# Kernel optimization log

Hardware: AMD Instinct MI355X
Metric: run time of the kernel (lower is better)

Reference implementation:

```python
import jax, jax.numpy as jnp
import numpy as np
import math

PS = 8          # patch_size
OUT_C = 16      # out_channels
D_MODEL = 64
P_STATE = 32
BANDLIMIT = 1.0
STEP_SCALE = 1.0  # dt1 reference rate


def _ln(x, g, b, eps=1e-5):
    mu = jnp.mean(x, -1, keepdims=True)
    var = jnp.mean((x - mu) ** 2, -1, keepdims=True)
    return (x - mu) * jax.lax.rsqrt(var + eps) * g + b


def _forward(x, W_embed, b_embed, g1, beta1, Lambda_re, Lambda_im, B_re, B_im,
             C_re, C_im, D, log_step, g2, beta2, W_enc, W_dec, g3, beta3, W_out, b_out):
    b, t, h, w = x.shape
    hp, wp = h // PS, w // PS
    n = hp * wp
    # patchify: [b,t,h,w] -> [b,t,n,ps*ps]
    xp = x.reshape(b, t, hp, PS, wp, PS).transpose(0, 1, 2, 4, 3, 5).reshape(b, t, n, PS * PS)
    xe = xp @ W_embed.T + b_embed                              # [b,t,n,d]
    u = xe.transpose(0, 2, 1, 3).reshape(b * n, t, D_MODEL)    # [(b n), t, d]

    # ---- S5Block: pre-norm -> diagonal SSM -> gelu + residual -> GEGLU FFN ----
    fx = _ln(u, g1, beta1)
    Lam = Lambda_re + 1j * Lambda_im                           # [P] complex eigenvalues
    step = STEP_SCALE * jnp.exp(log_step)                      # [P]
    Lbar = jnp.exp(Lam * step)                                 # ZOH: A_bar
    Bbar = ((Lbar - 1.0) / Lam)[:, None] * (B_re + 1j * B_im)  # ZOH: B_bar [P,d]
    # bandlimit mask on C (freqs = step*|Im(Lambda)|/(2pi) < bandlimit/2)
    freqs = step * jnp.abs(Lambda_im) / (2.0 * math.pi)
    mask = (freqs < BANDLIMIT * 0.5).astype(C_re.dtype)
    Cc = (C_re + 1j * C_im) * mask[None, :]                    # [d,P]

    Bu = jnp.einsum('ntd,pd->ntp', fx.astype(jnp.complex64), Bbar)   # [(bn),t,P]
    A = jnp.broadcast_to(Lbar.astype(jnp.complex64), (1, t, P_STATE))

    def comb(e1, e2):
        a1, b1 = e1
        a2, b2 = e2
        return a1 * a2, a2 * b1 + b2

    _, xs = jax.lax.associative_scan(comb, (A, Bu), axis=1)    # x_k = A*x_{k-1} + Bu_k (x_0 = 0)
    ys = jnp.einsum('ntp,dp->ntd', xs, Cc).real + fx * D       # y = Re(C x) + D u
    xb = jax.nn.gelu(ys, approximate=False) + fx

    fx2 = _ln(xb, g2, beta2)
    enc = fx2 @ W_enc.T                                        # [(bn),t,2d]
    a, gate = jnp.split(enc, 2, axis=-1)
    xb = (a * jax.nn.gelu(gate, approximate=False)) @ W_dec.T + fx2

    # ---- take last timestep, project, unpatchify ----
    x_last = xb[:, -1, :]                                      # [(bn), d]
    proj = _ln(x_last, g3, beta3) @ W_out.T + b_out            # [(bn), C*ps*ps]
    y = proj.reshape(b, hp, wp, OUT_C, PS, PS).transpose(0, 3, 1, 4, 2, 5).reshape(b, OUT_C, h, w)
    return y


def setup_inputs() -> dict:
    key = jax.random.key(0)
    ks = jax.random.split(key, 12)
    d, P, pp = D_MODEL, P_STATE, PS * PS
    return dict(
        x=jax.random.normal(ks[0], (8, 15, 480, 640), jnp.float32),
        W_embed=jax.random.normal(ks[1], (d, pp), jnp.float32) / math.sqrt(pp),
        b_embed=jnp.zeros((d,), jnp.float32),
        g1=jnp.ones((d,), jnp.float32), beta1=jnp.zeros((d,), jnp.float32),
        Lambda_re=-0.5 * jnp.ones((P,), jnp.float32),
        Lambda_im=math.pi * (1.0 + jnp.arange(P, dtype=jnp.float32)),
        B_re=jax.random.normal(ks[2], (P, d), jnp.float32) / math.sqrt(d),
        B_im=jax.random.normal(ks[3], (P, d), jnp.float32) / math.sqrt(d),
        C_re=jax.random.normal(ks[4], (d, P), jnp.float32) / math.sqrt(P),
        C_im=jax.random.normal(ks[5], (d, P), jnp.float32) / math.sqrt(P),
        D=jax.random.normal(ks[6], (d,), jnp.float32),
        log_step=jax.random.uniform(ks[7], (P,), jnp.float32, math.log(1e-3), math.log(1e-1)),
        g2=jnp.ones((d,), jnp.float32), beta2=jnp.zeros((d,), jnp.float32),
        W_enc=jax.random.normal(ks[8], (2 * d, d), jnp.float32) / math.sqrt(d),
        W_dec=jax.random.normal(ks[9], (d, d), jnp.float32) / math.sqrt(d),
        g3=jnp.ones((d,), jnp.float32), beta3=jnp.zeros((d,), jnp.float32),
        W_out=jax.random.normal(ks[10], (OUT_C * pp, d), jnp.float32) / math.sqrt(d),
        b_out=jnp.zeros((OUT_C * pp,), jnp.float32),
    )


def reference(x, W_embed, b_embed, g1, beta1, Lambda_re, Lambda_im, B_re, B_im,
              C_re, C_im, D, log_step, g2, beta2, W_enc, W_dec, g3, beta3, W_out, b_out):
    return _forward(x, W_embed, b_embed, g1, beta1, Lambda_re, Lambda_im, B_re, B_im,
                    C_re, C_im, D, log_step, g2, beta2, W_enc, W_dec, g3, beta3, W_out, b_out)
```

## Files before the change

kernel.cpp:

```cpp
#include <hip/hip_runtime.h>
#include <math.h>


typedef __attribute__((ext_vector_type(8))) short short8;
typedef __attribute__((ext_vector_type(4))) float f32x4;

#define MFMA16(a, b, c) __builtin_amdgcn_mfma_f32_16x16x32_bf16((a), (b), (c), 0, 0, 0)

__device__ __forceinline__ short f2bf(float f) {
  union { float f; unsigned u; } v; v.f = f;
  unsigned r = (v.u + 0x7fffu + ((v.u >> 16) & 1u)) >> 16;
  return (short)r;
}
__device__ __forceinline__ float geluf(float x) {
  return 0.5f * x * (1.0f + erff(x * 0.70710678118654752f));
}
__device__ __forceinline__ short8 packfrag(const f32x4& a, const f32x4& b) {
  short8 o;
  o[0] = f2bf(a[0]); o[1] = f2bf(a[1]); o[2] = f2bf(a[2]); o[3] = f2bf(a[3]);
  o[4] = f2bf(b[0]); o[5] = f2bf(b[1]); o[6] = f2bf(b[2]); o[7] = f2bf(b[3]);
  return o;
}
__device__ __forceinline__ int ecmap(int i, int m) {
  return (i >> 1) * 32 + (m >> 2) * 8 + (i & 1) * 4 + (m & 3);
}
__device__ __forceinline__ void bbar_factors(const float* Lre, const float* Lim,
                                             const float* lstep, int p,
                                             float& fre, float& fim) {
  float st = expf(lstep[p]);
  float lr = Lre[p], li = Lim[p];
  float er = expf(lr * st);
  float lbr = er * cosf(li * st), lbi = er * sinf(li * st);
  float u = lbr - 1.0f, v = lbi;
  float den = lr * lr + li * li;
  fre = (u * lr + v * li) / den;
  fim = (v * lr - u * li) / den;
}

__global__ __launch_bounds__(256) void k0_prep(
    const float* __restrict__ W_embed, const float* __restrict__ g1,
    const float* __restrict__ be1, const float* __restrict__ Lre,
    const float* __restrict__ Lim, const float* __restrict__ Bre,
    const float* __restrict__ Bim, const float* __restrict__ Cre,
    const float* __restrict__ Cim, const float* __restrict__ lstep,
    const float* __restrict__ W_enc, const float* __restrict__ W_dec,
    const float* __restrict__ W_out, short* __restrict__ wimg,
    float* __restrict__ bu0) {
  const int bid = blockIdx.x;
  if (bid == 44) {
    int q = threadIdx.x;
    if (q < 64) {
      int c = q >> 5, p = q & 31;
      float fre, fim; bbar_factors(Lre, Lim, lstep, p, fre, fim);
      float s = 0.f;
      for (int d = 0; d < 64; ++d) {
        float br = Bre[p * 64 + d], bi = Bim[p * 64 + d];
        float val = c ? (fre * bi + fim * br) : (fre * br - fim * bi);
        s += be1[d] * val;
      }
      bu0[q] = s;
    }
    return;
  }
  const int w = threadIdx.x >> 6, lane = threadIdx.x & 63;
  const int m = lane & 15, qd = lane >> 4;
  const int f = bid * 4 + w;
  short v[8];
  if (f < 8) {
    int i = f >> 1, kt = f & 1, chan = ecmap(i, m), k0 = kt * 32 + qd * 8;
#pragma unroll
    for (int j = 0; j < 8; ++j) v[j] = f2bf(W_embed[chan * 64 + k0 + j]);
  } else if (f < 16) {
    int fi = f - 8, i = fi >> 1, kt = fi & 1;
    int comp = i & 1, p = (i >> 1) * 16 + m, d0 = kt * 32 + qd * 8;
    float fre, fim; bbar_factors(Lre, Lim, lstep, p, fre, fim);
#pragma unroll
    for (int j = 0; j < 8; ++j) {
      int d = d0 + j;
      float br = Bre[p * 64 + d], bi = Bim[p * 64 + d];
      float val = comp ? (fre * bi + fim * br) : (fre * br - fim * bi);
      v[j] = f2bf(g1[d] * val);
    }
  } else if (f < 24) {
    int fi = f - 16, i = fi >> 1, kt = fi & 1, chan = ecmap(i, m);
#pragma unroll
    for (int j = 0; j < 8; ++j) {
      int comp = j >> 2, p = kt * 16 + qd * 4 + (j & 3);
      float stp = expf(lstep[p]);
      float fr = stp * fabsf(Lim[p]) * (1.0f / 6.28318530717958648f);
      float msk = (fr < 0.5f) ? 1.f : 0.f;
      float val = comp ? -Cim[chan * 32 + p] * msk : Cre[chan * 32 + p] * msk;
      v[j] = f2bf(val);
    }
  } else if (f < 40) {
    int fi = f - 24, i = fi >> 1, kt = fi & 1;
    int row = (i < 4) ? ecmap(i, m) : 64 + ecmap(i - 4, m);
#pragma unroll
    for (int j = 0; j < 8; ++j) v[j] = f2bf(W_enc[row * 64 + kt * 32 + qd * 8 + j]);
  } else if (f < 48) {
    int fi = f - 40, i = fi >> 1, kt = fi & 1, row = ecmap(i, m);
#pragma unroll
    for (int j = 0; j < 8; ++j) v[j] = f2bf(W_dec[row * 64 + kt * 32 + qd * 8 + j]);
  } else {
    int fi = f - 48, i = fi >> 1, kt = fi & 1, row = i * 16 + m;
#pragma unroll
    for (int j = 0; j < 8; ++j) v[j] = f2bf(W_out[row * 64 + kt * 32 + qd * 8 + j]);
  }
  short8 sv;
#pragma unroll
  for (int j = 0; j < 8; ++j) sv[j] = v[j];
  *(short8*)&wimg[(f * 64 + lane) * 8] = sv;
}

__global__ __launch_bounds__(256) void k1_fused(
    const float* __restrict__ x, const short* __restrict__ wimg_g,
    const float* __restrict__ bu0_g, const float* __restrict__ Lre,
    const float* __restrict__ Lim, const float* __restrict__ lstep,
    const float* __restrict__ g1, const float* __restrict__ be1,
    const float* __restrict__ bemb, const float* __restrict__ Dv,
    const float* __restrict__ g2, const float* __restrict__ be2,
    float* __restrict__ xlastT) {
  __shared__ short wimg[48 * 512];
  {
    float4* dst = (float4*)wimg;
    const float4* src = (const float4*)wimg_g;
    for (int i = threadIdx.x; i < 3072; i += 256) dst[i] = src[i];
  }
  __syncthreads();
#define WF(id) (*(const short8*)&wimg[(id) * 512 + lane * 8])

  const int wv = threadIdx.x >> 6, lane = threadIdx.x & 63;
  const int s = lane & 15, qd = lane >> 4;
  const int sbase = (blockIdx.x * 4 + wv) * 16;
  const int b_i = sbase / 4800;
  const int pr = sbase % 4800;
  const int ph = pr / 80;
  const int pw0 = pr % 80;
  const float* xbase = x + ((b_i * 15) * 480 + ph * 8) * 640 + (pw0 + s) * 8;

  int cb[4];
  f32x4 bec[4], bu0c[4];
#pragma unroll
  for (int nt = 0; nt < 4; ++nt) {
    cb[nt] = (nt >> 1) * 32 + qd * 8 + (nt & 1) * 4;
    bec[nt] = *(const f32x4*)(bemb + cb[nt]);
    bu0c[nt] = *(const f32x4*)(bu0_g + (nt & 1) * 32 + (nt >> 1) * 16 + qd * 4);
  }
  f32x4 lbr[2], lbi[2];
#pragma unroll
  for (int k = 0; k < 2; ++k)
#pragma unroll
    for (int r = 0; r < 4; ++r) {
      int p = k * 16 + qd * 4 + r;
      float st = expf(lstep[p]);
      float er = expf(Lre[p] * st);
      lbr[k][r] = er * cosf(Lim[p] * st);
      lbi[k][r] = er * sinf(Lim[p] * st);
    }

  const f32x4 zf = {0.f, 0.f, 0.f, 0.f};
  f32x4 state[4] = {zf, zf, zf, zf};
  f32x4 xh[4];

  f32x4 vcur[4], vnext[4];
#pragma unroll
  for (int kt = 0; kt < 2; ++kt) {
    const float* rp = xbase + (kt * 4 + qd) * 640;
    vcur[kt * 2] = *(const f32x4*)rp;
    vcur[kt * 2 + 1] = *(const f32x4*)(rp + 4);
  }

  for (int t = 0; t < 15; ++t) {
    if (t < 14) {
      const float* xn = xbase + (t + 1) * 307200;
#pragma unroll
      for (int kt = 0; kt < 2; ++kt) {
        const float* rp = xn + (kt * 4 + qd) * 640;
        vnext[kt * 2] = *(const f32x4*)rp;
        vnext[kt * 2 + 1] = *(const f32x4*)(rp + 4);
      }
    }
    short8 pa0 = packfrag(vcur[0], vcur[1]);
    short8 pa1 = packfrag(vcur[2], vcur[3]);
    f32x4 c1[4];
#pragma unroll
    for (int i = 0; i < 4; ++i) {
      f32x4 acc = MFMA16(WF(i * 2), pa0, zf);
      acc = MFMA16(WF(i * 2 + 1), pa1, acc);
      c1[i] = acc + bec[i];
    }
    float sm = 0.f, sq = 0.f;
#pragma unroll
    for (int nt = 0; nt < 4; ++nt)
#pragma unroll
      for (int i = 0; i < 4; ++i) { sm += c1[nt][i]; sq += c1[nt][i] * c1[nt][i]; }
    sm += __shfl_xor(sm, 16); sq += __shfl_xor(sq, 16);
    sm += __shfl_xor(sm, 32); sq += __shfl_xor(sq, 32);
    float mean = sm * 0.015625f;
    float rstd = rsqrtf(sq * 0.015625f - mean * mean + 1e-5f);
#pragma unroll
    for (int nt = 0; nt < 4; ++nt) xh[nt] = (c1[nt] - mean) * rstd;
    short8 xa0 = packfrag(xh[0], xh[1]);
    short8 xa1 = packfrag(xh[2], xh[3]);
#pragma unroll
    for (int k = 0; k < 2; ++k) {
      f32x4 re = state[2 * k], im = state[2 * k + 1];
      state[2 * k]     = lbr[k] * re - lbi[k] * im + bu0c[2 * k];
      state[2 * k + 1] = lbr[k] * im + lbi[k] * re + bu0c[2 * k + 1];
    }
#pragma unroll
    for (int i = 0; i < 4; ++i) {
      state[i] = MFMA16(WF(8 + i * 2), xa0, state[i]);
      state[i] = MFMA16(WF(8 + i * 2 + 1), xa1, state[i]);
    }
#pragma unroll
    for (int q = 0; q < 4; ++q) vcur[q] = vnext[q];
  }

  f32x4 g1c[4], b1c[4], Dc[4], g2c[4], b2c[4];
#pragma unroll
  for (int nt = 0; nt < 4; ++nt) {
    g1c[nt] = *(const f32x4*)(g1 + cb[nt]);
    b1c[nt] = *(const f32x4*)(be1 + cb[nt]);
    Dc[nt] = *(const f32x4*)(Dv + cb[nt]);
    g2c[nt] = *(const f32x4*)(g2 + cb[nt]);
    b2c[nt] = *(const f32x4*)(be2 + cb[nt]);
  }
  f32x4 fxl[4];
#pragma unroll
  for (int nt = 0; nt < 4; ++nt) fxl[nt] = xh[nt] * g1c[nt] + b1c[nt];

  short8 xsa0 = packfrag(state[0], state[1]);
  short8 xsa1 = packfrag(state[2], state[3]);
  f32x4 xbv[4];
#pragma unroll
  for (int i = 0; i < 4; ++i) {
    f32x4 acc = fxl[i] * Dc[i];
    acc = MFMA16(WF(16 + i * 2), xsa0, acc);
    acc = MFMA16(WF(16 + i * 2 + 1), xsa1, acc);
#pragma unroll
    for (int r = 0; r < 4; ++r) xbv[i][r] = geluf(acc[r]) + fxl[i][r];
  }
  float sm2 = 0.f, sq2 = 0.f;
#pragma unroll
  for (int nt = 0; nt < 4; ++nt)
#pragma unroll
    for (int i = 0; i < 4; ++i) { sm2 += xbv[nt][i]; sq2 += xbv[nt][i] * xbv[nt][i]; }
  sm2 += __shfl_xor(sm2, 16); sq2 += __shfl_xor(sq2, 16);
  sm2 += __shfl_xor(sm2, 32); sq2 += __shfl_xor(sq2, 32);
  float mean2 = sm2 * 0.015625f;
  float rstd2 = rsqrtf(sq2 * 0.015625f - mean2 * mean2 + 1e-5f);
  f32x4 fx2[4];
#pragma unroll
  for (int nt = 0; nt < 4; ++nt)
    fx2[nt] = (xbv[nt] - mean2) * rstd2 * g2c[nt] + b2c[nt];

  short8 fa0 = packfrag(fx2[0], fx2[1]);
  short8 fa1 = packfrag(fx2[2], fx2[3]);
  f32x4 e[8];
#pragma unroll
  for (int i = 0; i < 8; ++i) {
    f32x4 acc = MFMA16(WF(24 + i * 2), fa0, zf);
    e[i] = MFMA16(WF(24 + i * 2 + 1), fa1, acc);
  }
  f32x4 hv[4];
#pragma unroll
  for (int nt = 0; nt < 4; ++nt)
#pragma unroll
    for (int i = 0; i < 4; ++i) hv[nt][i] = e[nt][i] * geluf(e[nt + 4][i]);

  short8 ha0 = packfrag(hv[0], hv[1]);
  short8 ha1 = packfrag(hv[2], hv[3]);
  f32x4 xo[4];
#pragma unroll
  for (int i = 0; i < 4; ++i) {
    f32x4 acc = fx2[i];
    acc = MFMA16(WF(40 + i * 2), ha0, acc);
    xo[i] = MFMA16(WF(40 + i * 2 + 1), ha1, acc);
  }
#pragma unroll
  for (int kt = 0; kt < 2; ++kt)
#pragma unroll
    for (int j = 0; j < 8; ++j)
      xlastT[(kt * 32 + qd * 8 + j) * 38400 + sbase + s] = xo[2 * kt + (j >> 2)][j & 3];
#undef WF
}

__global__ __launch_bounds__(256) void k2_head(
    const float* __restrict__ xlastT, const short* __restrict__ wout_img,
    const float* __restrict__ g3, const float* __restrict__ be3,
    const float* __restrict__ b_out, float* __restrict__ y) {
  __shared__ short wo[32 * 512];
  const int nqb = blockIdx.x & 3;
  const int mblk = blockIdx.x >> 2;
  {
    float4* dst = (float4*)wo;
    const float4* src = (const float4*)(wout_img + nqb * 32 * 512);
    for (int i = threadIdx.x; i < 2048; i += 256) dst[i] = src[i];
  }
  __syncthreads();
  const int wv = threadIdx.x >> 6, lane = threadIdx.x & 63;
  const int s = lane & 15, qd = lane >> 4;
  const int sbase = mblk * 64 + wv * 16;
  const int seq = sbase + s;
  const int nq0 = nqb * 256;

  float vals[2][8];
#pragma unroll
  for (int kt = 0; kt < 2; ++kt)
#pragma unroll
    for (int j = 0; j < 8; ++j)
      vals[kt][j] = xlastT[(kt * 32 + qd * 8 + j) * 38400 + seq];
  float sm = 0.f, sq = 0.f;
#pragma unroll
  for (int kt = 0; kt < 2; ++kt)
#pragma unroll
    for (int j = 0; j < 8; ++j) { sm += vals[kt][j]; sq += vals[kt][j] * vals[kt][j]; }
  sm += __shfl_xor(sm, 16); sq += __shfl_xor(sq, 16);
  sm += __shfl_xor(sm, 32); sq += __shfl_xor(sq, 32);
  float mean = sm * 0.015625f;
  float rstd = rsqrtf(sq * 0.015625f - mean * mean + 1e-5f);

  short8 zb[2];
#pragma unroll
  for (int kt = 0; kt < 2; ++kt) {
    f32x4 ga = *(const f32x4*)(g3 + kt * 32 + qd * 8);
    f32x4 gb = *(const f32x4*)(g3 + kt * 32 + qd * 8 + 4);
    f32x4 ba = *(const f32x4*)(be3 + kt * 32 + qd * 8);
    f32x4 bb = *(const f32x4*)(be3 + kt * 32 + qd * 8 + 4);
#pragma unroll
    for (int j = 0; j < 4; ++j) {
      zb[kt][j] = f2bf((vals[kt][j] - mean) * rstd * ga[j] + ba[j]);
      zb[kt][j + 4] = f2bf((vals[kt][j + 4] - mean) * rstd * gb[j] + bb[j]);
    }
  }
  const int bi2 = seq / 4800, prr = seq % 4800;
  const int phh = prr / 80, pww = prr % 80;
  const int obase = (bi2 * 16 * 480 + phh * 8) * 640 + pww * 8;

#pragma unroll
  for (int nt = 0; nt < 16; ++nt) {
    int o0 = nq0 + nt * 16 + qd * 4;
    f32x4 acc = *(const f32x4*)(b_out + o0);
    acc = MFMA16(*(const short8*)&wo[(nt * 2 + 0) * 512 + lane * 8], zb[0], acc);
    acc = MFMA16(*(const short8*)&wo[(nt * 2 + 1) * 512 + lane * 8], zb[1], acc);
    int c = o0 >> 6, pi = (o0 >> 3) & 7, pj = o0 & 7;
    *(f32x4*)&y[obase + c * 307200 + pi * 640 + pj] = acc;
  }
}

extern "C" void kernel_launch(void* const* d_in, const int* in_sizes, int n_in,
                              void* d_out, int out_size, void* d_ws, size_t ws_size,
                              hipStream_t stream) {
  const float* x       = (const float*)d_in[0];
  const float* W_embed = (const float*)d_in[1];
  const float* b_embed = (const float*)d_in[2];
  const float* g1      = (const float*)d_in[3];
  const float* beta1   = (const float*)d_in[4];
  const float* Lre     = (const float*)d_in[5];
  const float* Lim     = (const float*)d_in[6];
  const float* Bre     = (const float*)d_in[7];
  const float* Bim     = (const float*)d_in[8];
  const float* Cre     = (const float*)d_in[9];
  const float* Cim     = (const float*)d_in[10];
  const float* Dv      = (const float*)d_in[11];
  const float* lstep   = (const float*)d_in[12];
  const float* g2      = (const float*)d_in[13];
  const float* beta2   = (const float*)d_in[14];
  const float* W_enc   = (const float*)d_in[15];
  const float* W_dec   = (const float*)d_in[16];
  const float* g3      = (const float*)d_in[17];
  const float* beta3   = (const float*)d_in[18];
  const float* W_out   = (const float*)d_in[19];
  const float* b_out   = (const float*)d_in[20];
  float* y = (float*)d_out;

  short* wimg = (short*)d_ws;
  float* bu0 = (float*)((char*)d_ws + 176 * 1024);
  float* xlastT = (float*)((char*)d_ws + 180 * 1024);

  k0_prep<<<dim3(45), dim3(256), 0, stream>>>(W_embed, g1, beta1, Lre, Lim,
                                              Bre, Bim, Cre, Cim, lstep,
                                              W_enc, W_dec, W_out, wimg, bu0);
  k1_fused<<<dim3(600), dim3(256), 0, stream>>>(x, wimg, bu0, Lre, Lim, lstep,
                                                g1, beta1, b_embed, Dv, g2,
                                                beta2, xlastT);
  k2_head<<<dim3(2400), dim3(256), 0, stream>>>(xlastT, wimg + 48 * 512, g3,
                                                beta3, b_out, y);
}
```

Baseline: 352.2 us.

## Split SSM time scan across waves and fuse final layernorm into k1

```diff
diff --git a/kernel.cpp b/kernel.cpp
--- a/kernel.cpp
+++ b/kernel.cpp
@@ -1,4 +1,5 @@
 #include <hip/hip_runtime.h>
+#include <hip/hip_bf16.h>
 #include <math.h>
 
 
@@ -12,14 +13,19 @@
   unsigned r = (v.u + 0x7fffu + ((v.u >> 16) & 1u)) >> 16;
   return (short)r;
 }
+__device__ __forceinline__ void pkpair(short8& o, int i, float a, float b) {
+  union { __hip_bfloat162 h; short s[2]; } u;
+  u.h = __float22bfloat162_rn(float2{a, b});
+  o[i] = u.s[0]; o[i + 1] = u.s[1];
+}
+__device__ __forceinline__ short8 packfrag(const f32x4& a, const f32x4& b) {
+  short8 o;
+  pkpair(o, 0, a[0], a[1]); pkpair(o, 2, a[2], a[3]);
+  pkpair(o, 4, b[0], b[1]); pkpair(o, 6, b[2], b[3]);
+  return o;
+}
 __device__ __forceinline__ float geluf(float x) {
   return 0.5f * x * (1.0f + erff(x * 0.70710678118654752f));
-}
-__device__ __forceinline__ short8 packfrag(const f32x4& a, const f32x4& b) {
-  short8 o;
-  o[0] = f2bf(a[0]); o[1] = f2bf(a[1]); o[2] = f2bf(a[2]); o[3] = f2bf(a[3]);
-  o[4] = f2bf(b[0]); o[5] = f2bf(b[1]); o[6] = f2bf(b[2]); o[7] = f2bf(b[3]);
-  return o;
 }
 __device__ __forceinline__ int ecmap(int i, int m) {
   return (i >> 1) * 32 + (m >> 2) * 8 + (i & 1) * 4 + (m & 3);
@@ -116,27 +122,32 @@
     const float* __restrict__ x, const short* __restrict__ wimg_g,
     const float* __restrict__ bu0_g, const float* __restrict__ Lre,
     const float* __restrict__ Lim, const float* __restrict__ lstep,
-    const float* __restrict__ g1, const float* __restrict__ be1,
-    const float* __restrict__ bemb, const float* __restrict__ Dv,
+    const float* __restrict__ bemb, const float* __restrict__ g1,
+    const float* __restrict__ be1, const float* __restrict__ Dv,
     const float* __restrict__ g2, const float* __restrict__ be2,
-    float* __restrict__ xlastT) {
-  __shared__ short wimg[48 * 512];
+    const float* __restrict__ g3, const float* __restrict__ be3,
+    short* __restrict__ zbuf) {
+  __shared__ short wlds[16 * 512];
+  __shared__ float part[3 * 16 * 64];
   {
-    float4* dst = (float4*)wimg;
+    float4* dst = (float4*)wlds;
     const float4* src = (const float4*)wimg_g;
-    for (int i = threadIdx.x; i < 3072; i += 256) dst[i] = src[i];
+    for (int i = threadIdx.x; i < 1024; i += 256) dst[i] = src[i];
   }
   __syncthreads();
-#define WF(id) (*(const short8*)&wimg[(id) * 512 + lane * 8])
+#define WF(id) (*(const short8*)&wlds[(id) * 512 + lane * 8])
+#define GF(id) (*(const short8*)&wimg_g[(id) * 512 + lane * 8])
 
   const int wv = threadIdx.x >> 6, lane = threadIdx.x & 63;
   const int s = lane & 15, qd = lane >> 4;
-  const int sbase = (blockIdx.x * 4 + wv) * 16;
+  const int sbase = blockIdx.x * 16;
   const int b_i = sbase / 4800;
   const int pr = sbase % 4800;
   const int ph = pr / 80;
   const int pw0 = pr % 80;
-  const float* xbase = x + ((b_i * 15) * 480 + ph * 8) * 640 + (pw0 + s) * 8;
+  const int t0 = wv * 4, tn = (wv == 3) ? 3 : 4;
+  const float* xbase =
+      x + ((b_i * 15 + t0) * 480 + ph * 8) * 640 + (pw0 + s) * 8;
 
   int cb[4];
   f32x4 bec[4], bu0c[4];
@@ -170,9 +181,9 @@
     vcur[kt * 2 + 1] = *(const f32x4*)(rp + 4);
   }
 
-  for (int t = 0; t < 15; ++t) {
-    if (t < 14) {
-      const float* xn = xbase + (t + 1) * 307200;
+  for (int it = 0; it < tn; ++it) {
+    if (it + 1 < tn) {
+      const float* xn = xbase + (it + 1) * 307200;
 #pragma unroll
       for (int kt = 0; kt < 2; ++kt) {
         const float* rp = xn + (kt * 4 + qd) * 640;
@@ -216,6 +227,45 @@
 #pragma unroll
     for (int q = 0; q < 4; ++q) vcur[q] = vnext[q];
   }
+
+  short8 cc2f[8];
+  if (wv < 3) {
+    int e = 11 - wv * 4;
+    f32x4 pwr[2], pwi[2];
+#pragma unroll
+    for (int k = 0; k < 2; ++k) { pwr[k] = lbr[k]; pwi[k] = lbi[k]; }
+    for (int it = 1; it < e; ++it)
+#pragma unroll
+      for (int k = 0; k < 2; ++k) {
+        f32x4 nr = pwr[k] * lbr[k] - pwi[k] * lbi[k];
+        f32x4 ni = pwr[k] * lbi[k] + pwi[k] * lbr[k];
+        pwr[k] = nr; pwi[k] = ni;
+      }
+#pragma unroll
+    for (int k = 0; k < 2; ++k) {
+      f32x4 re = state[2 * k], im = state[2 * k + 1];
+      state[2 * k]     = pwr[k] * re - pwi[k] * im;
+      state[2 * k + 1] = pwr[k] * im + pwi[k] * re;
+    }
+#pragma unroll
+    for (int i = 0; i < 4; ++i)
+#pragma unroll
+      for (int r = 0; r < 4; ++r)
+        part[((wv * 16 + i * 4 + r) << 6) + lane] = state[i][r];
+  } else {
+#pragma unroll
+    for (int i = 0; i < 8; ++i) cc2f[i] = GF(16 + i);
+  }
+  __syncthreads();
+  if (wv != 3) return;
+
+#pragma unroll
+  for (int w = 0; w < 3; ++w)
+#pragma unroll
+    for (int i = 0; i < 4; ++i)
+#pragma unroll
+      for (int r = 0; r < 4; ++r)
+        state[i][r] += part[((w * 16 + i * 4 + r) << 6) + lane];
 
   f32x4 g1c[4], b1c[4], Dc[4], g2c[4], b2c[4];
 #pragma unroll
@@ -236,8 +286,8 @@
 #pragma unroll
   for (int i = 0; i < 4; ++i) {
     f32x4 acc = fxl[i] * Dc[i];
-    acc = MFMA16(WF(16 + i * 2), xsa0, acc);
-    acc = MFMA16(WF(16 + i * 2 + 1), xsa1, acc);
+    acc = MFMA16(cc2f[i * 2], xsa0, acc);
+    acc = MFMA16(cc2f[i * 2 + 1], xsa1, acc);
 #pragma unroll
     for (int r = 0; r < 4; ++r) xbv[i][r] = geluf(acc[r]) + fxl[i][r];
   }
@@ -259,9 +309,15 @@
   short8 fa1 = packfrag(fx2[2], fx2[3]);
   f32x4 e[8];
 #pragma unroll
-  for (int i = 0; i < 8; ++i) {
-    f32x4 acc = MFMA16(WF(24 + i * 2), fa0, zf);
-    e[i] = MFMA16(WF(24 + i * 2 + 1), fa1, acc);
+  for (int half = 0; half < 2; ++half) {
+    short8 ef[8];
+#pragma unroll
+    for (int i = 0; i < 8; ++i) ef[i] = GF(24 + half * 8 + i);
+#pragma unroll
+    for (int i = 0; i < 4; ++i) {
+      f32x4 acc = MFMA16(ef[i * 2], fa0, zf);
+      e[half * 4 + i] = MFMA16(ef[i * 2 + 1], fa1, acc);
+    }
   }
   f32x4 hv[4];
 #pragma unroll
@@ -269,26 +325,45 @@
 #pragma unroll
     for (int i = 0; i < 4; ++i) hv[nt][i] = e[nt][i] * geluf(e[nt + 4][i]);
 
+  short8 df[8];
+#pragma unroll
+  for (int i = 0; i < 8; ++i) df[i] = GF(40 + i);
   short8 ha0 = packfrag(hv[0], hv[1]);
   short8 ha1 = packfrag(hv[2], hv[3]);
   f32x4 xo[4];
 #pragma unroll
   for (int i = 0; i < 4; ++i) {
     f32x4 acc = fx2[i];
-    acc = MFMA16(WF(40 + i * 2), ha0, acc);
-    xo[i] = MFMA16(WF(40 + i * 2 + 1), ha1, acc);
-  }
-#pragma unroll
-  for (int kt = 0; kt < 2; ++kt)
-#pragma unroll
-    for (int j = 0; j < 8; ++j)
-      xlastT[(kt * 32 + qd * 8 + j) * 38400 + sbase + s] = xo[2 * kt + (j >> 2)][j & 3];
+    acc = MFMA16(df[i * 2], ha0, acc);
+    xo[i] = MFMA16(df[i * 2 + 1], ha1, acc);
+  }
+
+  float sm3 = 0.f, sq3 = 0.f;
+#pragma unroll
+  for (int nt = 0; nt < 4; ++nt)
+#pragma unroll
+    for (int i = 0; i < 4; ++i) { sm3 += xo[nt][i]; sq3 += xo[nt][i] * xo[nt][i]; }
+  sm3 += __shfl_xor(sm3, 16); sq3 += __shfl_xor(sq3, 16);
+  sm3 += __shfl_xor(sm3, 32); sq3 += __shfl_xor(sq3, 32);
+  float mean3 = sm3 * 0.015625f;
+  float rstd3 = rsqrtf(sq3 * 0.015625f - mean3 * mean3 + 1e-5f);
+  f32x4 z[4];
+#pragma unroll
+  for (int nt = 0; nt < 4; ++nt) {
+    f32x4 g3c = *(const f32x4*)(g3 + cb[nt]);
+    f32x4 b3c = *(const f32x4*)(be3 + cb[nt]);
+    z[nt] = (xo[nt] - mean3) * rstd3 * g3c + b3c;
+  }
+  short8 z0 = packfrag(z[0], z[1]);
+  short8 z1 = packfrag(z[2], z[3]);
+  *(short8*)&zbuf[(sbase + s) * 64 + qd * 8] = z0;
+  *(short8*)&zbuf[(sbase + s) * 64 + 32 + qd * 8] = z1;
 #undef WF
+#undef GF
 }
 
 __global__ __launch_bounds__(256) void k2_head(
-    const float* __restrict__ xlastT, const short* __restrict__ wout_img,
-    const float* __restrict__ g3, const float* __restrict__ be3,
+    const short* __restrict__ zbuf, const short* __restrict__ wout_img,
     const float* __restrict__ b_out, float* __restrict__ y) {
   __shared__ short wo[32 * 512];
   const int nqb = blockIdx.x & 3;
@@ -298,42 +373,15 @@
     const float4* src = (const float4*)(wout_img + nqb * 32 * 512);
     for (int i = threadIdx.x; i < 2048; i += 256) dst[i] = src[i];
   }
-  __syncthreads();
   const int wv = threadIdx.x >> 6, lane = threadIdx.x & 63;
   const int s = lane & 15, qd = lane >> 4;
   const int sbase = mblk * 64 + wv * 16;
   const int seq = sbase + s;
   const int nq0 = nqb * 256;
-
-  float vals[2][8];
-#pragma unroll
-  for (int kt = 0; kt < 2; ++kt)
-#pragma unroll
-    for (int j = 0; j < 8; ++j)
-      vals[kt][j] = xlastT[(kt * 32 + qd * 8 + j) * 38400 + seq];
-  float sm = 0.f, sq = 0.f;
-#pragma unroll
-  for (int kt = 0; kt < 2; ++kt)
-#pragma unroll
-    for (int j = 0; j < 8; ++j) { sm += vals[kt][j]; sq += vals[kt][j] * vals[kt][j]; }
-  sm += __shfl_xor(sm, 16); sq += __shfl_xor(sq, 16);
-  sm += __shfl_xor(sm, 32); sq += __shfl_xor(sq, 32);
-  float mean = sm * 0.015625f;
-  float rstd = rsqrtf(sq * 0.015625f - mean * mean + 1e-5f);
-
-  short8 zb[2];
-#pragma unroll
-  for (int kt = 0; kt < 2; ++kt) {
-    f32x4 ga = *(const f32x4*)(g3 + kt * 32 + qd * 8);
-    f32x4 gb = *(const f32x4*)(g3 + kt * 32 + qd * 8 + 4);
-    f32x4 ba = *(const f32x4*)(be3 + kt * 32 + qd * 8);
-    f32x4 bb = *(const f32x4*)(be3 + kt * 32 + qd * 8 + 4);
-#pragma unroll
-    for (int j = 0; j < 4; ++j) {
-      zb[kt][j] = f2bf((vals[kt][j] - mean) * rstd * ga[j] + ba[j]);
-      zb[kt][j + 4] = f2bf((vals[kt][j + 4] - mean) * rstd * gb[j] + bb[j]);
-    }
-  }
+  short8 zb0 = *(const short8*)&zbuf[seq * 64 + qd * 8];
+  short8 zb1 = *(const short8*)&zbuf[seq * 64 + 32 + qd * 8];
+  __syncthreads();
+
   const int bi2 = seq / 4800, prr = seq % 4800;
   const int phh = prr / 80, pww = prr % 80;
   const int obase = (bi2 * 16 * 480 + phh * 8) * 640 + pww * 8;
@@ -342,8 +390,8 @@
   for (int nt = 0; nt < 16; ++nt) {
     int o0 = nq0 + nt * 16 + qd * 4;
     f32x4 acc = *(const f32x4*)(b_out + o0);
-    acc = MFMA16(*(const short8*)&wo[(nt * 2 + 0) * 512 + lane * 8], zb[0], acc);
-    acc = MFMA16(*(const short8*)&wo[(nt * 2 + 1) * 512 + lane * 8], zb[1], acc);
+    acc = MFMA16(*(const short8*)&wo[(nt * 2 + 0) * 512 + lane * 8], zb0, acc);
+    acc = MFMA16(*(const short8*)&wo[(nt * 2 + 1) * 512 + lane * 8], zb1, acc);
     int c = o0 >> 6, pi = (o0 >> 3) & 7, pj = o0 & 7;
     *(f32x4*)&y[obase + c * 307200 + pi * 640 + pj] = acc;
   }
@@ -377,14 +425,13 @@
 
   short* wimg = (short*)d_ws;
   float* bu0 = (float*)((char*)d_ws + 176 * 1024);
-  float* xlastT = (float*)((char*)d_ws + 180 * 1024);
+  short* zbuf = (short*)((char*)d_ws + 180 * 1024);
 
   k0_prep<<<dim3(45), dim3(256), 0, stream>>>(W_embed, g1, beta1, Lre, Lim,
                                               Bre, Bim, Cre, Cim, lstep,
                                               W_enc, W_dec, W_out, wimg, bu0);
-  k1_fused<<<dim3(600), dim3(256), 0, stream>>>(x, wimg, bu0, Lre, Lim, lstep,
-                                                g1, beta1, b_embed, Dv, g2,
-                                                beta2, xlastT);
-  k2_head<<<dim3(2400), dim3(256), 0, stream>>>(xlastT, wimg + 48 * 512, g3,
-                                                beta3, b_out, y);
-}
+  k1_fused<<<dim3(2400), dim3(256), 0, stream>>>(x, wimg, bu0, Lre, Lim, lstep,
+                                                 b_embed, g1, beta1, Dv, g2,
+                                                 beta2, g3, beta3, zbuf);
+  k2_head<<<dim3(2400), dim3(256), 0, stream>>>(zbuf, wimg + 48 * 512, b_out, y);
+}
```

Result: no change. 352.5 us (+0.1%).
